# Kernel optimization log

Hardware: AMD Instinct MI355X
Metric: run time of the kernel (lower is better)

Reference implementation:

```python
import jax, jax.numpy as jnp
import numpy as np
from jax import lax

B, UNITS, IN_DIM = 1024, 4096, 256
CHI = 4  # forced: scatter writes 16 = chi*chi values per pair


def setup_inputs() -> dict:
    key = jax.random.key(0)
    k1, k2, k3 = jax.random.split(key, 3)
    inputs = jax.random.normal(k1, (B, IN_DIM), dtype=jnp.float32)
    W = jax.random.normal(k2, (UNITS, IN_DIM), dtype=jnp.float32) * 0.5  # sigma=0.5
    b = 2.0 * jnp.pi * jax.random.uniform(k3, (UNITS,), dtype=jnp.float32)
    return {"inputs": inputs, "W": W, "b": b}


def reference(inputs, W, b):
    # theta: [B, U]
    theta = inputs @ W.T + b
    half = theta * 0.5
    c = jnp.cos(half) ** 2          # R00 (real)
    s = jnp.sin(half) ** 2          # R11 (real)
    o = jnp.sin(theta) * 0.5        # imag part of R01
    z = jnp.zeros_like(c)
    R00 = lax.complex(c, z)
    R01 = lax.complex(z, o)
    R10 = lax.complex(z, -o)
    R11 = lax.complex(s, z)
    # R: [B, U, 2, 2] single-qubit rotation matrix per unit
    R = jnp.stack([jnp.stack([R00, R01], -1), jnp.stack([R10, R11], -1)], -2)
    A = R[:, 0::2]   # [B, K, 2, 2], K = U/2
    Bm = R[:, 1::2]  # [B, K, 2, 2]
    # kron(A, Bm)[2a+c, 2b+d] = A[a,b] * Bm[c,d] -> axes (a,c,b,d) then reshape
    kron = (A[:, :, :, None, :, None] * Bm[:, :, None, :, None, :]).reshape(
        A.shape[0], A.shape[1], CHI, CHI)
    # original returns (batch, chi, chi, units/2)
    return jnp.transpose(kron, (0, 2, 3, 1))
```

## Files before the change

### kernel.cpp

```cpp
#include <hip/hip_runtime.h>

#define IND 256
#define KC  32

__global__ __launch_bounds__(256, 4)
void FeatureEncodingLayer_30374008718005_kernel(
        const float* __restrict__ X,
        const float* __restrict__ W,
        const float* __restrict__ bias,
        float* __restrict__ outf)
{
    __shared__ float Ws[2][KC][128];

    const int tid  = threadIdx.x;
    const int lane = tid & 63;
    const int wid  = __builtin_amdgcn_readfirstlane(tid >> 6);

    const int ut = blockIdx.x & 31;
    const int bt = blockIdx.x >> 5;
    const int b0 = bt * 32;
    const int u0 = ut * 128;
    const int p0 = ut * 64;

    const int q  = tid & 7;
    const int rq = tid >> 3;

    const float* xw = X + (size_t)(b0 + 8 * wid) * IND;

    float acc[8][2];
#pragma unroll
    for (int i = 0; i < 8; ++i) { acc[i][0] = 0.f; acc[i][1] = 0.f; }

    float4 pf[4];
#define STAGE_LOAD(c) do {                                                     \
    _Pragma("unroll")                                                          \
    for (int j = 0; j < 4; ++j)                                                \
        pf[j] = *reinterpret_cast<const float4*>(                              \
            W + (size_t)(u0 + rq + 32 * j) * IND + (c) * KC + q * 4);          \
    } while (0)

#define STAGE_WRITE(buf) do {                                                  \
    _Pragma("unroll")                                                          \
    for (int j = 0; j < 4; ++j) {                                              \
        const int col = (rq + 32 * j) ^ (q << 2);                              \
        Ws[buf][q * 4 + 0][col] = pf[j].x;                                     \
        Ws[buf][q * 4 + 1][col] = pf[j].y;                                     \
        Ws[buf][q * 4 + 2][col] = pf[j].z;                                     \
        Ws[buf][q * 4 + 3][col] = pf[j].w;                                     \
    }                                                                          \
    } while (0)

    STAGE_LOAD(0);
    STAGE_WRITE(0);
    __syncthreads();

    for (int c = 0; c < IND / KC; ++c) {
        const int cur = c & 1;
        if (c < IND / KC - 1) STAGE_LOAD(c + 1);

        {
            const int zrc = (int)((0xEDB87421u >> (4 * c)) & 0xFu);
            float* zp = outf + (size_t)(b0 + 8 * wid) * 32768
                       + (size_t)zrc * 2048 + p0 + lane;
#pragma unroll
            for (int i = 0; i < 8; ++i)
                zp[(size_t)i * 32768] = 0.f;
        }

        const float* xc = xw + c * KC;
#pragma unroll 4
        for (int k = 0; k < KC; ++k) {
            const int s = ((k >> 2) & 7) << 2;
            const float2 wv = *reinterpret_cast<const float2*>(
                &Ws[cur][k][(2 * lane) ^ s]);
#pragma unroll
            for (int i = 0; i < 8; ++i) {
                const float xv = xc[i * IND + k];
                acc[i][0] = fmaf(xv, wv.x, acc[i][0]);
                acc[i][1] = fmaf(xv, wv.y, acc[i][1]);
            }
        }
        if (c < IND / KC - 1) {
            STAGE_WRITE(cur ^ 1);
            __syncthreads();
        }
    }
#undef STAGE_LOAD
#undef STAGE_WRITE

    const float2 bv = *reinterpret_cast<const float2*>(bias + u0 + 2 * lane);

#pragma unroll
    for (int i = 0; i < 8; ++i) {
        const int b = b0 + 8 * wid + i;
        const float tA = acc[i][0] + bv.x;
        const float tB = acc[i][1] + bv.y;
        float sA, cA, sB, cB;
        __sincosf(tA, &sA, &cA);
        __sincosf(tB, &sB, &cB);
        const float ca = 0.5f * (1.f + cA);
        const float sa = 0.5f * (1.f - cA);
        const float cb = 0.5f * (1.f + cB);
        const float sb = 0.5f * (1.f - cB);
        const float oo = 0.25f * sA * sB;

        float* bp = outf + (size_t)b * 32768 + p0 + lane;
        bp[ 0 * 2048] =  ca * cb;
        bp[ 3 * 2048] = -oo;
        bp[ 5 * 2048] =  ca * sb;
        bp[ 6 * 2048] =  oo;
        bp[ 9 * 2048] =  oo;
        bp[10 * 2048] =  sa * cb;
        bp[12 * 2048] = -oo;
        bp[15 * 2048] =  sa * sb;
    }
}

extern "C" void kernel_launch(void* const* d_in, const int* in_sizes, int n_in,
                              void* d_out, int out_size, void* d_ws, size_t ws_size,
                              hipStream_t stream) {
    const float* X  = (const float*)d_in[0];
    const float* W  = (const float*)d_in[1];
    const float* bv = (const float*)d_in[2];

    FeatureEncodingLayer_30374008718005_kernel<<<dim3(1024), dim3(256), 0, stream>>>(
        X, W, bv, (float*)d_out);
}
```

Measured before the change: 47.08 us.

## Enlarge block tile to 128 batch rows with 64-wide K chunks and unrolled pipeline

Each block now covers 128 batch rows with 512 threads, and each wave computes 16 rows instead of 8. W is staged in 64-wide K chunks, stored in a paired-k swizzled layout so each lane reads float4s. The K loop is fully unrolled into four stages. The zero-fill stores move out of the compute loop and go out in one batch before the last compute stage. The aim is more reuse of each staged W tile and fewer syncs, at the cost of more registers, far fewer blocks (256), and one block per CU by launch bounds.

```diff
diff --git a/kernel.cpp b/kernel.cpp
--- a/kernel.cpp
+++ b/kernel.cpp
@@ -1,16 +1,16 @@
 #include <hip/hip_runtime.h>
 
 #define IND 256
-#define KC  32
+#define KC  64
 
-__global__ __launch_bounds__(256, 4)
+__global__ __launch_bounds__(512, 1)
 void FeatureEncodingLayer_30374008718005_kernel(
         const float* __restrict__ X,
         const float* __restrict__ W,
         const float* __restrict__ bias,
         float* __restrict__ outf)
 {
-    __shared__ float Ws[2][KC][128];
+    __shared__ float Ws[2][KC / 2][256];
 
     const int tid  = threadIdx.x;
     const int lane = tid & 63;
@@ -18,18 +18,18 @@
 
     const int ut = blockIdx.x & 31;
     const int bt = blockIdx.x >> 5;
-    const int b0 = bt * 32;
+    const int b0 = bt * 128 + 16 * wid;
     const int u0 = ut * 128;
     const int p0 = ut * 64;
 
-    const int q  = tid & 7;
-    const int rq = tid >> 3;
+    const int q  = tid & 15;
+    const int rq = tid >> 4;
 
-    const float* xw = X + (size_t)(b0 + 8 * wid) * IND;
+    const float* xc = X + (size_t)b0 * IND;
 
-    float acc[8][2];
+    float acc[16][2];
 #pragma unroll
-    for (int i = 0; i < 8; ++i) { acc[i][0] = 0.f; acc[i][1] = 0.f; }
+    for (int i = 0; i < 16; ++i) { acc[i][0] = 0.f; acc[i][1] = 0.f; }
 
     float4 pf[4];
 #define STAGE_LOAD(c) do {                                                     \
@@ -40,59 +40,65 @@
     } while (0)
 
 #define STAGE_WRITE(buf) do {                                                  \
+    const int kp0 = 2 * q, kp1 = 2 * q + 1;                                    \
+    const int sw0 = (kp0 & 7) << 2, sw1 = (kp1 & 7) << 2;                      \
     _Pragma("unroll")                                                          \
     for (int j = 0; j < 4; ++j) {                                              \
-        const int col = (rq + 32 * j) ^ (q << 2);                              \
-        Ws[buf][q * 4 + 0][col] = pf[j].x;                                     \
-        Ws[buf][q * 4 + 1][col] = pf[j].y;                                     \
-        Ws[buf][q * 4 + 2][col] = pf[j].z;                                     \
-        Ws[buf][q * 4 + 3][col] = pf[j].w;                                     \
+        const int u2 = 2 * (rq + 32 * j);                                      \
+        *reinterpret_cast<float2*>(&Ws[buf][kp0][u2 ^ sw0]) =                  \
+            make_float2(pf[j].x, pf[j].y);                                     \
+        *reinterpret_cast<float2*>(&Ws[buf][kp1][u2 ^ sw1]) =                  \
+            make_float2(pf[j].z, pf[j].w);                                     \
     }                                                                          \
     } while (0)
 
-    STAGE_LOAD(0);
-    STAGE_WRITE(0);
-    __syncthreads();
+#define COMPUTE(buf, c) do {                                                   \
+    _Pragma("unroll")                                                          \
+    for (int t = 0; t < 16; ++t) {                                             \
+        const int sw0 = ((2 * t) & 7) << 2, sw1 = ((2 * t + 1) & 7) << 2;      \
+        const float4 w0 = *reinterpret_cast<const float4*>(                    \
+            &Ws[buf][2 * t][(4 * lane) ^ sw0]);                                \
+        const float4 w1 = *reinterpret_cast<const float4*>(                    \
+            &Ws[buf][2 * t + 1][(4 * lane) ^ sw1]);                            \
+        _Pragma("unroll")                                                      \
+        for (int i = 0; i < 16; ++i) {                                         \
+            const float4 xv = *reinterpret_cast<const float4*>(                \
+                xc + i * IND + (c) * KC + 4 * t);                              \
+            acc[i][0] = fmaf(xv.x, w0.x, acc[i][0]);                           \
+            acc[i][0] = fmaf(xv.y, w0.y, acc[i][0]);                           \
+            acc[i][1] = fmaf(xv.x, w0.z, acc[i][1]);                           \
+            acc[i][1] = fmaf(xv.y, w0.w, acc[i][1]);                           \
+            acc[i][0] = fmaf(xv.z, w1.x, acc[i][0]);                           \
+            acc[i][0] = fmaf(xv.w, w1.y, acc[i][0]);                           \
+            acc[i][1] = fmaf(xv.z, w1.z, acc[i][1]);                           \
+            acc[i][1] = fmaf(xv.w, w1.w, acc[i][1]);                           \
+        }                                                                      \
+    }                                                                          \
+    } while (0)
 
-    for (int c = 0; c < IND / KC; ++c) {
-        const int cur = c & 1;
-        if (c < IND / KC - 1) STAGE_LOAD(c + 1);
+    STAGE_LOAD(0); STAGE_WRITE(0); __syncthreads();
+    STAGE_LOAD(1); COMPUTE(0, 0); STAGE_WRITE(1); __syncthreads();
+    STAGE_LOAD(2); COMPUTE(1, 1); STAGE_WRITE(0); __syncthreads();
+    STAGE_LOAD(3); COMPUTE(0, 2); STAGE_WRITE(1); __syncthreads();
 
-        {
-            const int zrc = (int)((0xEDB87421u >> (4 * c)) & 0xFu);
-            float* zp = outf + (size_t)(b0 + 8 * wid) * 32768
-                       + (size_t)zrc * 2048 + p0 + lane;
 #pragma unroll
-            for (int i = 0; i < 8; ++i)
-                zp[(size_t)i * 32768] = 0.f;
-        }
+    for (int i = 0; i < 16; ++i) {
+        float* zb = outf + (size_t)(b0 + i) * 32768 + p0 + lane;
+        zb[ 1 * 2048] = 0.f; zb[ 2 * 2048] = 0.f;
+        zb[ 4 * 2048] = 0.f; zb[ 7 * 2048] = 0.f;
+        zb[ 8 * 2048] = 0.f; zb[11 * 2048] = 0.f;
+        zb[13 * 2048] = 0.f; zb[14 * 2048] = 0.f;
+    }
 
-        const float* xc = xw + c * KC;
-#pragma unroll 4
-        for (int k = 0; k < KC; ++k) {
-            const int s = ((k >> 2) & 7) << 2;
-            const float2 wv = *reinterpret_cast<const float2*>(
-                &Ws[cur][k][(2 * lane) ^ s]);
-#pragma unroll
-            for (int i = 0; i < 8; ++i) {
-                const float xv = xc[i * IND + k];
-                acc[i][0] = fmaf(xv, wv.x, acc[i][0]);
-                acc[i][1] = fmaf(xv, wv.y, acc[i][1]);
-            }
-        }
-        if (c < IND / KC - 1) {
-            STAGE_WRITE(cur ^ 1);
-            __syncthreads();
-        }
-    }
+    COMPUTE(1, 3);
 #undef STAGE_LOAD
 #undef STAGE_WRITE
+#undef COMPUTE
 
     const float2 bv = *reinterpret_cast<const float2*>(bias + u0 + 2 * lane);
 
 #pragma unroll
-    for (int i = 0; i < 8; ++i) {
-        const int b = b0 + 8 * wid + i;
+    for (int i = 0; i < 16; ++i) {
         const float tA = acc[i][0] + bv.x;
         const float tB = acc[i][1] + bv.y;
         float sA, cA, sB, cB;
@@ -104,7 +110,7 @@
         const float sb = 0.5f * (1.f - cB);
         const float oo = 0.25f * sA * sB;
 
-        float* bp = outf + (size_t)b * 32768 + p0 + lane;
+        float* bp = outf + (size_t)(b0 + i) * 32768 + p0 + lane;
         bp[ 0 * 2048] =  ca * cb;
         bp[ 3 * 2048] = -oo;
         bp[ 5 * 2048] =  ca * sb;
@@ -123,6 +129,6 @@
     const float* W  = (const float*)d_in[1];
     const float* bv = (const float*)d_in[2];
 
-    FeatureEncodingLayer_30374008718005_kernel<<<dim3(1024), dim3(256), 0, stream>>>(
+    FeatureEncodingLayer_30374008718005_kernel<<<dim3(256), dim3(512), 0, stream>>>(
         X, W, bv, (float*)d_out);
 }
```

After: 116.0 us. +146.4%, slower.

## Enlarge batch tile to 64 rows and load W in two half-K stages

Applied to the files above, without the earlier changes.

Each block now covers 64 batch rows (16 per wave) instead of 32, so each W tile is reused over twice as many rows and the grid halves to 512 blocks. The K dimension is loaded in two 128-wide shared-memory stages with no double buffering, and the zero stores to the off-diagonal outputs are issued in one batch during the second stage. In exchange the kernel uses 64KB of LDS and more accumulator registers per thread, with occupancy reduced to 2 blocks per CU, and global loads no longer overlap with compute.

```diff
diff --git a/kernel.cpp b/kernel.cpp
--- a/kernel.cpp
+++ b/kernel.cpp
@@ -1,16 +1,15 @@
 #include <hip/hip_runtime.h>
 
 #define IND 256
-#define KC  32
 
-__global__ __launch_bounds__(256, 4)
+__global__ __launch_bounds__(256, 2)
 void FeatureEncodingLayer_30374008718005_kernel(
         const float* __restrict__ X,
         const float* __restrict__ W,
         const float* __restrict__ bias,
         float* __restrict__ outf)
 {
-    __shared__ float Ws[2][KC][128];
+    __shared__ float Ws[128][128];
 
     const int tid  = threadIdx.x;
     const int lane = tid & 63;
@@ -18,81 +17,73 @@
 
     const int ut = blockIdx.x & 31;
     const int bt = blockIdx.x >> 5;
-    const int b0 = bt * 32;
+    const int b0 = bt * 64 + 16 * wid;
     const int u0 = ut * 128;
     const int p0 = ut * 64;
 
-    const int q  = tid & 7;
-    const int rq = tid >> 3;
+    const int k4 = tid & 31;
+    const int ur = tid >> 5;
 
-    const float* xw = X + (size_t)(b0 + 8 * wid) * IND;
+    const float* xc = X + (size_t)b0 * IND;
 
-    float acc[8][2];
+    float acc[16][2];
 #pragma unroll
-    for (int i = 0; i < 8; ++i) { acc[i][0] = 0.f; acc[i][1] = 0.f; }
+    for (int i = 0; i < 16; ++i) { acc[i][0] = 0.f; acc[i][1] = 0.f; }
 
-    float4 pf[4];
-#define STAGE_LOAD(c) do {                                                     \
-    _Pragma("unroll")                                                          \
-    for (int j = 0; j < 4; ++j)                                                \
-        pf[j] = *reinterpret_cast<const float4*>(                              \
-            W + (size_t)(u0 + rq + 32 * j) * IND + (c) * KC + q * 4);          \
-    } while (0)
+#pragma unroll
+    for (int st = 0; st < 2; ++st) {
+        if (st) __syncthreads();
+#pragma unroll
+        for (int sp = 0; sp < 2; ++sp) {
+            float4 pf[8];
+#pragma unroll
+            for (int j = 0; j < 8; ++j) {
+                const int u = ur + 8 * (sp * 8 + j);
+                pf[j] = *reinterpret_cast<const float4*>(
+                    W + (size_t)(u0 + u) * IND + st * 128 + 4 * k4);
+            }
+            const int m = (k4 & 7) << 2;
+#pragma unroll
+            for (int j = 0; j < 8; ++j) {
+                const int col = (ur + 8 * (sp * 8 + j)) ^ m;
+                Ws[4 * k4 + 0][col] = pf[j].x;
+                Ws[4 * k4 + 1][col] = pf[j].y;
+                Ws[4 * k4 + 2][col] = pf[j].z;
+                Ws[4 * k4 + 3][col] = pf[j].w;
+            }
+        }
+        __syncthreads();
 
-#define STAGE_WRITE(buf) do {                                                  \
-    _Pragma("unroll")                                                          \
-    for (int j = 0; j < 4; ++j) {                                              \
-        const int col = (rq + 32 * j) ^ (q << 2);                              \
-        Ws[buf][q * 4 + 0][col] = pf[j].x;                                     \
-        Ws[buf][q * 4 + 1][col] = pf[j].y;                                     \
-        Ws[buf][q * 4 + 2][col] = pf[j].z;                                     \
-        Ws[buf][q * 4 + 3][col] = pf[j].w;                                     \
-    }                                                                          \
-    } while (0)
-
-    STAGE_LOAD(0);
-    STAGE_WRITE(0);
-    __syncthreads();
-
-    for (int c = 0; c < IND / KC; ++c) {
-        const int cur = c & 1;
-        if (c < IND / KC - 1) STAGE_LOAD(c + 1);
-
-        {
-            const int zrc = (int)((0xEDB87421u >> (4 * c)) & 0xFu);
-            float* zp = outf + (size_t)(b0 + 8 * wid) * 32768
-                       + (size_t)zrc * 2048 + p0 + lane;
+        if (st == 1) {
 #pragma unroll
-            for (int i = 0; i < 8; ++i)
-                zp[(size_t)i * 32768] = 0.f;
+            for (int i = 0; i < 16; ++i) {
+                float* zb = outf + (size_t)(b0 + i) * 32768 + p0 + lane;
+                zb[ 1 * 2048] = 0.f; zb[ 2 * 2048] = 0.f;
+                zb[ 4 * 2048] = 0.f; zb[ 7 * 2048] = 0.f;
+                zb[ 8 * 2048] = 0.f; zb[11 * 2048] = 0.f;
+                zb[13 * 2048] = 0.f; zb[14 * 2048] = 0.f;
+            }
         }
 
-        const float* xc = xw + c * KC;
 #pragma unroll 4
-        for (int k = 0; k < KC; ++k) {
-            const int s = ((k >> 2) & 7) << 2;
+        for (int kk = 0; kk < 128; ++kk) {
+            const int mm = ((kk >> 2) & 7) << 2;
             const float2 wv = *reinterpret_cast<const float2*>(
-                &Ws[cur][k][(2 * lane) ^ s]);
+                &Ws[kk][(2 * lane) ^ mm]);
+            const int kg = st * 128 + kk;
 #pragma unroll
-            for (int i = 0; i < 8; ++i) {
-                const float xv = xc[i * IND + k];
+            for (int i = 0; i < 16; ++i) {
+                const float xv = xc[i * IND + kg];
                 acc[i][0] = fmaf(xv, wv.x, acc[i][0]);
                 acc[i][1] = fmaf(xv, wv.y, acc[i][1]);
             }
         }
-        if (c < IND / KC - 1) {
-            STAGE_WRITE(cur ^ 1);
-            __syncthreads();
-        }
     }
-#undef STAGE_LOAD
-#undef STAGE_WRITE
 
     const float2 bv = *reinterpret_cast<const float2*>(bias + u0 + 2 * lane);
 
 #pragma unroll
-    for (int i = 0; i < 8; ++i) {
-        const int b = b0 + 8 * wid + i;
+    for (int i = 0; i < 16; ++i) {
         const float tA = acc[i][0] + bv.x;
         const float tB = acc[i][1] + bv.y;
         float sA, cA, sB, cB;
@@ -104,7 +95,7 @@
         const float sb = 0.5f * (1.f - cB);
         const float oo = 0.25f * sA * sB;
 
-        float* bp = outf + (size_t)b * 32768 + p0 + lane;
+        float* bp = outf + (size_t)(b0 + i) * 32768 + p0 + lane;
         bp[ 0 * 2048] =  ca * cb;
         bp[ 3 * 2048] = -oo;
         bp[ 5 * 2048] =  ca * sb;
@@ -123,6 +114,6 @@
     const float* W  = (const float*)d_in[1];
     const float* bv = (const float*)d_in[2];
 
-    FeatureEncodingLayer_30374008718005_kernel<<<dim3(1024), dim3(256), 0, stream>>>(
+    FeatureEncodingLayer_30374008718005_kernel<<<dim3(512), dim3(256), 0, stream>>>(
         X, W, bv, (float*)d_out);
 }
```

Result: slower. 55.92 us (+18.8%).

## Pack W pairs of k in LDS for float4 reads and lighter barrier

Applied to the files above, without the earlier changes.

Changes the shared-memory tile layout so that two consecutive k values for a pair of units sit adjacent, letting each lane read a float4 per two k steps instead of a float2 per step. Stores become float2 with a new XOR swizzle, and the X loads read two consecutive k values per iteration. __syncthreads is replaced by an explicit lgkmcnt wait plus s_barrier, which skips waiting on outstanding global memory operations. This halves the number of LDS read instructions, at the cost of a different bank-conflict pattern and reliance on correct manual synchronization.

```diff
diff --git a/kernel.cpp b/kernel.cpp
--- a/kernel.cpp
+++ b/kernel.cpp
@@ -10,7 +10,7 @@
         const float* __restrict__ bias,
         float* __restrict__ outf)
 {
-    __shared__ float Ws[2][KC][128];
+    __shared__ float Ws[2][KC / 2][256];
 
     const int tid  = threadIdx.x;
     const int lane = tid & 63;
@@ -25,7 +25,7 @@
     const int q  = tid & 7;
     const int rq = tid >> 3;
 
-    const float* xw = X + (size_t)(b0 + 8 * wid) * IND;
+    const float* xc = X + (size_t)(b0 + 8 * wid) * IND;
 
     float acc[8][2];
 #pragma unroll
@@ -40,19 +40,26 @@
     } while (0)
 
 #define STAGE_WRITE(buf) do {                                                  \
+    const int kp0 = 2 * q, kp1 = 2 * q + 1;                                    \
+    const int sw0 = (kp0 & 7) << 2, sw1 = (kp1 & 7) << 2;                      \
     _Pragma("unroll")                                                          \
     for (int j = 0; j < 4; ++j) {                                              \
-        const int col = (rq + 32 * j) ^ (q << 2);                              \
-        Ws[buf][q * 4 + 0][col] = pf[j].x;                                     \
-        Ws[buf][q * 4 + 1][col] = pf[j].y;                                     \
-        Ws[buf][q * 4 + 2][col] = pf[j].z;                                     \
-        Ws[buf][q * 4 + 3][col] = pf[j].w;                                     \
+        const int u2 = 2 * (rq + 32 * j);                                      \
+        *reinterpret_cast<float2*>(&Ws[buf][kp0][u2 ^ sw0]) =                  \
+            make_float2(pf[j].x, pf[j].y);                                     \
+        *reinterpret_cast<float2*>(&Ws[buf][kp1][u2 ^ sw1]) =                  \
+            make_float2(pf[j].z, pf[j].w);                                     \
     }                                                                          \
+    } while (0)
+
+#define LDS_BARRIER() do {                                                     \
+    asm volatile("s_waitcnt lgkmcnt(0)" ::: "memory");                         \
+    __builtin_amdgcn_s_barrier();                                              \
     } while (0)
 
     STAGE_LOAD(0);
     STAGE_WRITE(0);
-    __syncthreads();
+    LDS_BARRIER();
 
     for (int c = 0; c < IND / KC; ++c) {
         const int cur = c & 1;
@@ -67,26 +74,30 @@
                 zp[(size_t)i * 32768] = 0.f;
         }
 
-        const float* xc = xw + c * KC;
-#pragma unroll 4
-        for (int k = 0; k < KC; ++k) {
-            const int s = ((k >> 2) & 7) << 2;
-            const float2 wv = *reinterpret_cast<const float2*>(
-                &Ws[cur][k][(2 * lane) ^ s]);
+#pragma unroll 8
+        for (int kp = 0; kp < KC / 2; ++kp) {
+            const int sw = (kp & 7) << 2;
+            const float4 wq = *reinterpret_cast<const float4*>(
+                &Ws[cur][kp][(4 * lane) ^ sw]);
+            const int kg = c * KC + 2 * kp;
 #pragma unroll
             for (int i = 0; i < 8; ++i) {
-                const float xv = xc[i * IND + k];
-                acc[i][0] = fmaf(xv, wv.x, acc[i][0]);
-                acc[i][1] = fmaf(xv, wv.y, acc[i][1]);
+                const float x0 = xc[i * IND + kg];
+                const float x1 = xc[i * IND + kg + 1];
+                acc[i][0] = fmaf(x0, wq.x, acc[i][0]);
+                acc[i][0] = fmaf(x1, wq.y, acc[i][0]);
+                acc[i][1] = fmaf(x0, wq.z, acc[i][1]);
+                acc[i][1] = fmaf(x1, wq.w, acc[i][1]);
             }
         }
         if (c < IND / KC - 1) {
             STAGE_WRITE(cur ^ 1);
-            __syncthreads();
+            LDS_BARRIER();
         }
     }
 #undef STAGE_LOAD
 #undef STAGE_WRITE
+#undef LDS_BARRIER
 
     const float2 bv = *reinterpret_cast<const float2*>(bias + u0 + 2 * lane);
 
```

New measurement: 44.18 us. 6.1% less time.
